# Kernel tuning notes

Hardware: AMD Instinct MI355X
Metric: run time of the kernel (lower is better)

## Reference

```python
import jax, jax.numpy as jnp
import numpy as np
import math

B, S, OBS, ACT = 64, 256, 96, 29
D, H, L, FF = 512, 8, 8, 2048
HD = D // H
EPS = 1e-5

def _ln(x, g, b):
    m = jnp.mean(x, axis=-1, keepdims=True)
    v = jnp.mean((x - m) ** 2, axis=-1, keepdims=True)
    return (x - m) * jax.lax.rsqrt(v + EPS) * g + b

def _pos_encoding():
    pos = jnp.arange(S, dtype=jnp.float32)[:, None]
    div = jnp.exp(jnp.arange(0, D, 2, dtype=jnp.float32) * (-math.log(10000.0) / D))
    pe = jnp.zeros((S, D), dtype=jnp.float32)
    pe = pe.at[:, 0::2].set(jnp.sin(pos * div))
    pe = pe.at[:, 1::2].set(jnp.cos(pos * div))
    return pe

def setup_inputs() -> dict:
    key = jax.random.key(0)
    ks = iter(jax.random.split(key, 64))
    def w(shape, scale=0.02):
        return jax.random.normal(next(ks), shape, dtype=jnp.float32) * scale
    inp = {
        "observations": jax.random.normal(next(ks), (B, S, OBS), dtype=jnp.float32),
        "W_in": w((OBS, D)), "b_in": jnp.zeros((D,)),
        "g_in": jnp.ones((D,)), "be_in": jnp.zeros((D,)),
        "Wq": w((L, D, D)), "bq": jnp.zeros((L, D)),
        "Wk": w((L, D, D)), "bk": jnp.zeros((L, D)),
        "Wv": w((L, D, D)), "bv": jnp.zeros((L, D)),
        "Wo": w((L, D, D)), "bo": jnp.zeros((L, D)),
        "g1": jnp.ones((L, D)), "be1": jnp.zeros((L, D)),
        "W1": w((L, D, FF)), "b1": jnp.zeros((L, FF)),
        "W2": w((L, FF, D)), "b2": jnp.zeros((L, D)),
        "g2": jnp.ones((L, D)), "be2": jnp.zeros((L, D)),
        "Wp1": w((D, D // 2)), "bp1": jnp.zeros((D // 2,)),
        "gp1": jnp.ones((D // 2,)), "bep1": jnp.zeros((D // 2,)),
        "Wp2": w((D // 2, D // 4)), "bp2": jnp.zeros((D // 4,)),
        "gp2": jnp.ones((D // 4,)), "bep2": jnp.zeros((D // 4,)),
        "Wp3": w((D // 4, ACT)), "bp3": jnp.zeros((ACT,)),
        "action_scale": jnp.ones((ACT,)), "action_bias": jnp.zeros((ACT,)),
    }
    return inp

def _forward(observations, W_in, b_in, g_in, be_in, Wq, bq, Wk, bk, Wv, bv, Wo, bo,
             g1, be1, W1, b1, W2, b2, g2, be2,
             Wp1, bp1, gp1, bep1, Wp2, bp2, gp2, bep2, Wp3, bp3,
             action_scale, action_bias):
    gelu = lambda x: jax.nn.gelu(x, approximate=False)
    # input projection + LN + GELU (dropout = identity in eval)
    x = gelu(_ln(observations @ W_in + b_in, g_in, be_in))
    x = x + _pos_encoding()[None, :, :]  # [B,S,D]
    scale = 1.0 / math.sqrt(HD)
    for l in range(L):
        q = (x @ Wq[l] + bq[l]).reshape(B, S, H, HD)
        k = (x @ Wk[l] + bk[l]).reshape(B, S, H, HD)
        v = (x @ Wv[l] + bv[l]).reshape(B, S, H, HD)
        scores = jnp.einsum('bqhd,bkhd->bhqk', q, k) * scale
        attn = jax.nn.softmax(scores, axis=-1)
        o = jnp.einsum('bhqk,bkhd->bqhd', attn, v).reshape(B, S, D)
        x = _ln(x + (o @ Wo[l] + bo[l]), g1[l], be1[l])
        h = gelu(x @ W1[l] + b1[l])
        x = _ln(x + (h @ W2[l] + b2[l]), g2[l], be2[l])
    y = gelu(_ln(x @ Wp1 + bp1, gp1, bep1))
    y = gelu(_ln(y @ Wp2 + bp2, gp2, bep2))
    actions = jnp.tanh(y @ Wp3 + bp3)
    return actions * action_scale + action_bias

def reference(observations, W_in, b_in, g_in, be_in, Wq, bq, Wk, bk, Wv, bv, Wo, bo,
              g1, be1, W1, b1, W2, b2, g2, be2,
              Wp1, bp1, gp1, bep1, Wp2, bp2, gp2, bep2, Wp3, bp3,
              action_scale, action_bias):
    return _forward(observations, W_in, b_in, g_in, be_in, Wq, bq, Wk, bk, Wv, bv, Wo, bo,
                    g1, be1, W1, b1, W2, b2, g2, be2,
                    Wp1, bp1, gp1, bep1, Wp2, bp2, gp2, bep2, Wp3, bp3,
                    action_scale, action_bias)
```

## Files before the change

kernel.cpp:

```cpp
#include <hip/hip_runtime.h>

typedef unsigned short u16;
typedef unsigned int u32;
typedef __attribute__((ext_vector_type(8))) __bf16 bf16x8;
typedef __attribute__((ext_vector_type(4))) float f32x4;
typedef __attribute__((ext_vector_type(2))) float f32x2;

#define B_ 64
#define S_ 256
#define OBS_ 96
#define ACT_ 29
#define D_ 512
#define H_ 8
#define L_ 8
#define FF_ 2048
#define HD_ 64
#define NTOK (B_ * S_)
#define QKV3 (3 * D_)

__device__ __forceinline__ u16 f2bf(float f) {
    __bf16 h = (__bf16)f;
    u16 u; __builtin_memcpy(&u, &h, 2); return u;
}
__device__ __forceinline__ float bf2f(u16 h) {
    return __uint_as_float(((u32)h) << 16);
}
__device__ __forceinline__ u16 f2h(float f) {
    _Float16 h = (_Float16)f;
    u16 u; __builtin_memcpy(&u, &h, 2); return u;
}
__device__ __forceinline__ float h2f(u16 u) {
    _Float16 h; __builtin_memcpy(&h, &u, 2); return (float)h;
}
__device__ __forceinline__ float gelu_f(float x) {
    const float k1 = 2.3022121f;
    const float k2 = 0.10294451f;
    float x2 = x * x;
    float arg = x * __builtin_fmaf(x2, k2, k1);
    float e = exp2f(arg);
    float r = __builtin_amdgcn_rcpf(1.0f + e);
    return __builtin_fmaf(-x, r, x);
}
__device__ __forceinline__ f32x2 gelu2(f32x2 x) {
    const float k1 = 2.3022121f;
    const float k2 = 0.10294451f;
    f32x2 x2 = x * x;
    f32x2 arg = x * (x2 * k2 + k1);
    f32x2 e;
    e.x = exp2f(arg.x);
    e.y = exp2f(arg.y);
    f32x2 one_e = e + 1.0f;
    f32x2 r;
    r.x = __builtin_amdgcn_rcpf(one_e.x);
    r.y = __builtin_amdgcn_rcpf(one_e.y);
    return x - x * r;
}
__device__ __forceinline__ void gld_lds16(const u16* g, u16* l) {
    __builtin_amdgcn_global_load_lds(
        (const __attribute__((address_space(1))) unsigned int*)g,
        (__attribute__((address_space(3))) unsigned int*)l, 16, 0, 0);
}

__global__ __launch_bounds__(256) void transpose_bf16_kernel(
    const float* __restrict__ src, u16* __restrict__ dst, int K, int N,
    size_t srcStride, size_t dstStride)
{
    __shared__ float tile[32][33];
    int n0 = blockIdx.x * 32, k0 = blockIdx.y * 32;
    const float* s = src + (size_t)blockIdx.z * srcStride;
    u16* d = dst + (size_t)blockIdx.z * dstStride;
    int tx = threadIdx.x, ty = threadIdx.y;
    for (int i = 0; i < 32; i += 8)
        tile[ty + i][tx] = s[(size_t)(k0 + ty + i) * N + n0 + tx];
    __syncthreads();
    for (int i = 0; i < 32; i += 8)
        d[(size_t)(n0 + ty + i) * K + k0 + tx] = f2bf(tile[tx][ty + i]);
}

__global__ __launch_bounds__(256) void concat_bias_kernel(
    const float* __restrict__ bq, const float* __restrict__ bk,
    const float* __restrict__ bv, float* __restrict__ dst)
{
    int i = blockIdx.x * 256 + threadIdx.x;
    int l = i / QKV3, r = i - l * QKV3;
    float v;
    if (r < D_)            v = bq[l * D_ + r];
    else if (r < 2 * D_)   v = bk[l * D_ + r - D_];
    else                   v = bv[l * D_ + r - 2 * D_];
    dst[i] = v;
}

__global__ __launch_bounds__(256) void in_gemm_kernel(
    const float* __restrict__ obs, const float* __restrict__ Win,
    const float* __restrict__ b_in, float* __restrict__ outp)
{
    __shared__ float As[OBS_][68];
    __shared__ float Bs[OBS_][68];
    int m0 = blockIdx.y * 64, n0 = blockIdx.x * 64;
    int t = threadIdx.x;
    #pragma unroll
    for (int i = 0; i < 24; i++) {
        int idx = i * 256 + t;
        int m = idx / OBS_, kk = idx - m * OBS_;
        As[kk][m] = obs[(size_t)(m0 + m) * OBS_ + kk];
    }
    #pragma unroll
    for (int i = 0; i < 24; i++) {
        int idx = i * 256 + t;
        int kk = idx >> 6, n = idx & 63;
        Bs[kk][n] = Win[(size_t)kk * D_ + n0 + n];
    }
    __syncthreads();
    int tm = t >> 4, tn = t & 15;
    float acc[4][4] = {};
    for (int kk = 0; kk < OBS_; kk++) {
        float4 a = *(const float4*)&As[kk][tm * 4];
        float4 b = *(const float4*)&Bs[kk][tn * 4];
        const float av[4] = {a.x, a.y, a.z, a.w};
        const float bv[4] = {b.x, b.y, b.z, b.w};
        #pragma unroll
        for (int r = 0; r < 4; r++)
            #pragma unroll
            for (int c = 0; c < 4; c++) acc[r][c] += av[r] * bv[c];
    }
    #pragma unroll
    for (int r = 0; r < 4; r++)
        #pragma unroll
        for (int c = 0; c < 4; c++) {
            int col = n0 + tn * 4 + c;
            outp[(size_t)(m0 + tm * 4 + r) * D_ + col] = acc[r][c] + b_in[col];
        }
}

template <int EPI, int TN, bool SPLITK>
__global__ __launch_bounds__(256, 2) void gemm_bt_kernel(
    const u16* __restrict__ A, const u16* __restrict__ BT,
    const float* __restrict__ bias, void* __restrict__ C,
    void* __restrict__ C2, int M, int N, int K, int kLen)
{
    constexpr int NI = TN / 32;
    constexpr int NB = TN / 32;
    constexpr int BUFSZ = 128 * 64 + TN * 64;
    __shared__ __align__(16) u16 smem[2 * BUFSZ];
    int bx = blockIdx.x;
    int m0 = (bx & 127) * 128, n0 = (bx >> 7) * TN;
    int z = SPLITK ? blockIdx.z : 0;
    int kStart = z * kLen;
    int t = threadIdx.x;
    int lane = t & 63, w = t >> 6;
    int wm = w >> 1, wn = w & 1;
    int l15 = lane & 15, quad = lane >> 4;

    int offC[4]; int ci8[4];
    #pragma unroll
    for (int i = 0; i < 4; i++) {
        int ci = t + i * 256;
        int r = ci >> 3, s = ci & 7, gc = s ^ (r & 7);
        offC[i] = r * K + gc * 8;
        ci8[i] = ci * 8;
    }
    const u16* Abase = A + (size_t)m0 * K + kStart;
    const u16* Bbase = BT + (size_t)n0 * K + kStart;

    int aoff[2][4], boff[2][NI];
    #pragma unroll
    for (int kh = 0; kh < 2; kh++) {
        #pragma unroll
        for (int mi = 0; mi < 4; mi++) {
            int row = wm * 64 + mi * 16 + l15;
            aoff[kh][mi] = row * 64 + (((kh * 4 + quad) ^ (row & 7)) * 8);
        }
        #pragma unroll
        for (int ni = 0; ni < NI; ni++) {
            int row = wn * (TN / 2) + ni * 16 + l15;
            boff[kh][ni] = row * 64 + (((kh * 4 + quad) ^ (row & 7)) * 8);
        }
    }

    f32x4 acc[4][NI];
    f32x4 zero = {0.f, 0.f, 0.f, 0.f};
    #pragma unroll
    for (int mi = 0; mi < 4; mi++)
        #pragma unroll
        for (int ni = 0; ni < NI; ni++) acc[mi][ni] = zero;

    auto stage = [&](int buf, int kt) {
        const u16* Ab = Abase + kt * 64;
        const u16* Bb = Bbase + kt * 64;
        u16* dstA = smem + buf * BUFSZ;
        u16* dstB = dstA + 128 * 64;
        #pragma unroll
        for (int i = 0; i < 4; i++) gld_lds16(Ab + offC[i], dstA + ci8[i]);
        #pragma unroll
        for (int i = 0; i < NB; i++) gld_lds16(Bb + offC[i], dstB + ci8[i]);
    };

    int nk = kLen >> 6;
    stage(0, 0);
    for (int kt = 0; kt < nk; ++kt) {
        int cur = kt & 1;
        __syncthreads();
        if (kt + 1 < nk) stage(cur ^ 1, kt + 1);
        const u16* As = smem + cur * BUFSZ;
        const u16* Bs = As + 128 * 64;
        #pragma unroll
        for (int kh = 0; kh < 2; kh++) {
            bf16x8 a[4], b[NI];
            #pragma unroll
            for (int mi = 0; mi < 4; mi++)
                a[mi] = *(const bf16x8*)&As[aoff[kh][mi]];
            #pragma unroll
            for (int ni = 0; ni < NI; ni++)
                b[ni] = *(const bf16x8*)&Bs[boff[kh][ni]];
            #pragma unroll
            for (int mi = 0; mi < 4; mi++)
                #pragma unroll
                for (int ni = 0; ni < NI; ni++)
                    acc[mi][ni] = __builtin_amdgcn_mfma_f32_16x16x32_bf16(
                        a[mi], b[ni], acc[mi][ni], 0, 0, 0);
        }
    }

    bool partial = SPLITK && (z == 1);
    if (EPI == 2) {
        #pragma unroll
        for (int ni = 0; ni < NI; ni++) {
            int col = n0 + wn * (TN / 2) + ni * 16 + l15;
            float bv = partial ? 0.f : bias[col];
            #pragma unroll
            for (int mi = 0; mi < 4; mi++) {
                int rbase = m0 + wm * 64 + mi * 16 + quad * 4;
                f32x4 v = acc[mi][ni];
                #pragma unroll
                for (int r = 0; r < 4; r++)
                    ((float*)C)[(size_t)(rbase + r) * N + col] = v[r] + bv;
            }
        }
    } else {
        __syncthreads();
        u16* Ct = smem;
        #pragma unroll
        for (int ni = 0; ni < NI; ni++) {
            int colt = wn * (TN / 2) + ni * 16 + l15;
            float bv = partial ? 0.f : bias[n0 + colt];
            #pragma unroll
            for (int mi = 0; mi < 4; mi++) {
                int rbase = wm * 64 + mi * 16 + quad * 4;
                f32x4 v = acc[mi][ni];
                f32x2 y01 = {v[0], v[1]};
                f32x2 y23 = {v[2], v[3]};
                y01 = y01 + bv;
                y23 = y23 + bv;
                if (EPI == 1) { y01 = gelu2(y01); y23 = gelu2(y23); }
                const float ys[4] = {y01.x, y01.y, y23.x, y23.y};
                #pragma unroll
                for (int r = 0; r < 4; r++) {
                    u16 hv = (EPI == 3) ? f2h(ys[r]) : f2bf(ys[r]);
                    int row = rbase + r;
                    int cc = colt >> 3;
                    Ct[row * TN + (((cc ^ (row & 7)) * 8) | (colt & 7))] = hv;
                }
            }
        }
        __syncthreads();
        u16* dst = partial ? (u16*)C2 : (u16*)C;
        constexpr int CPR = TN / 8;
        #pragma unroll
        for (int i = 0; i < TN / 16; i++) {
            int ch = t + i * 256;
            int row = ch / CPR, cc = ch % CPR;
            uint4 vv = *(const uint4*)&Ct[row * TN + ((cc ^ (row & 7)) * 8)];
            *(uint4*)(dst + (size_t)(m0 + row) * N + n0 + cc * 8) = vv;
        }
    }
}

__global__ __launch_bounds__(256) void attn_kernel(
    const u16* __restrict__ qkv, u16* __restrict__ o)
{
    __shared__ __align__(16) u16 kvs[S_ * HD_];
    __shared__ __align__(16) u16 P[4 * 16 * S_];
    int bx = blockIdx.x;
    int qc = bx & 3;
    int h = (bx >> 2) & 7;
    int b = bx >> 5;
    int t = threadIdx.x;
    int lane = t & 63, w = t >> 6;
    int l15 = lane & 15, quad = lane >> 4;
    size_t rowb = (size_t)b * S_;

    {
        const u16* src = qkv + (rowb + t) * QKV3 + D_ + h * HD_;
        int sw = t & 7;
        #pragma unroll
        for (int j = 0; j < 8; j++)
            *(uint4*)&kvs[t * HD_ + ((j ^ sw) * 8)] = *(const uint4*)(src + j * 8);
    }
    bf16x8 aQ[2];
    {
        int qrow = qc * 64 + w * 16 + l15;
        const u16* src = qkv + (rowb + qrow) * QKV3 + h * HD_ + quad * 8;
        aQ[0] = *(const bf16x8*)(src);
        aQ[1] = *(const bf16x8*)(src + 32);
    }
    __syncthreads();

    f32x4 sc[16];
    #pragma unroll
    for (int nc = 0; nc < 16; nc++) {
        f32x4 acc = {0.f, 0.f, 0.f, 0.f};
        int row = nc * 16 + l15;
        int s0 = quad ^ (row & 7);
        bf16x8 b0 = *(const bf16x8*)&kvs[row * HD_ + s0 * 8];
        bf16x8 b1 = *(const bf16x8*)&kvs[row * HD_ + (s0 ^ 4) * 8];
        acc = __builtin_amdgcn_mfma_f32_16x16x32_bf16(aQ[0], b0, acc, 0, 0, 0);
        acc = __builtin_amdgcn_mfma_f32_16x16x32_bf16(aQ[1], b1, acc, 0, 0, 0);
        sc[nc] = acc;
    }
    const float scale = 0.125f;
    float rmax[4], rinv[4];
    #pragma unroll
    for (int r = 0; r < 4; r++) {
        float mx = -1e30f;
        #pragma unroll
        for (int nc = 0; nc < 16; nc++) mx = fmaxf(mx, sc[nc][r]);
        for (int off = 1; off < 16; off <<= 1) mx = fmaxf(mx, __shfl_xor(mx, off));
        rmax[r] = mx * scale;
    }
    #pragma unroll
    for (int r = 0; r < 4; r++) {
        float sum = 0.f;
        #pragma unroll
        for (int nc = 0; nc < 16; nc++) {
            float p = __expf(sc[nc][r] * scale - rmax[r]);
            sc[nc][r] = p;
            sum += p;
        }
        for (int off = 1; off < 16; off <<= 1) sum += __shfl_xor(sum, off);
        rinv[r] = 1.0f / sum;
    }
    #pragma unroll
    for (int nc = 0; nc < 16; nc++)
        #pragma unroll
        for (int r = 0; r < 4; r++) {
            int prow = quad * 4 + r;
            int col = nc * 16 + l15;
            int slot = (col >> 3) ^ (prow & 7);
            P[w * 4096 + prow * 256 + slot * 8 + (col & 7)] = f2bf(sc[nc][r]);
        }
    __syncthreads();

    {
        const u16* src = qkv + (rowb + t) * QKV3 + 2 * D_ + h * HD_;
        int chunkc = t >> 3, bytec = t & 7;
        #pragma unroll
        for (int dj = 0; dj < 8; dj++) {
            uint4 x = *(const uint4*)(src + dj * 8);
            const u16* xs = (const u16*)&x;
            #pragma unroll
            for (int i = 0; i < 8; i++) {
                int vrow = dj * 8 + i;
                kvs[vrow * 256 + ((chunkc ^ (vrow & 7)) * 8) + bytec] = xs[i];
            }
        }
    }
    __syncthreads();

    f32x4 accO[4];
    f32x4 zero = {0.f, 0.f, 0.f, 0.f};
    #pragma unroll
    for (int nt = 0; nt < 4; nt++) accO[nt] = zero;
    for (int ks = 0; ks < 8; ks++) {
        int ch = ks * 4 + quad;
        bf16x8 aP = *(const bf16x8*)&P[w * 4096 + l15 * 256 + ((ch ^ (l15 & 7)) * 8)];
        #pragma unroll
        for (int nt = 0; nt < 4; nt++) {
            int vrow = nt * 16 + l15;
            bf16x8 bV = *(const bf16x8*)&kvs[vrow * 256 + ((ch ^ (vrow & 7)) * 8)];
            accO[nt] = __builtin_amdgcn_mfma_f32_16x16x32_bf16(aP, bV, accO[nt], 0, 0, 0);
        }
    }
    __syncthreads();
    u16* Ot = P;
    #pragma unroll
    for (int nt = 0; nt < 4; nt++)
        #pragma unroll
        for (int r = 0; r < 4; r++) {
            int row = w * 16 + quad * 4 + r;
            int col = nt * 16 + l15;
            int cc = col >> 3;
            Ot[row * 64 + (((cc ^ (row & 7)) * 8) | (col & 7))] =
                f2bf(accO[nt][r] * rinv[r]);
        }
    __syncthreads();
    #pragma unroll
    for (int i = 0; i < 2; i++) {
        int ch = t + i * 256;
        int row = ch >> 3, cc = ch & 7;
        uint4 vv = *(const uint4*)&Ot[row * 64 + ((cc ^ (row & 7)) * 8)];
        *(uint4*)(o + (rowb + qc * 64 + row) * D_ + h * HD_ + cc * 8) = vv;
    }
}

template <int WIDTH, int INK, bool RES, bool GELU, bool PE, bool SUM2>
__global__ __launch_bounds__(256) void ln_kernel(
    const void* __restrict__ in, const void* __restrict__ in2,
    const u16* __restrict__ res,
    const float* __restrict__ g, const float* __restrict__ b,
    u16* __restrict__ out)
{
    constexpr int T = WIDTH / 4;
    constexpr int R = 256 / T;
    __shared__ float rs[R][2], rq[R][2];
    int t = threadIdx.x;
    int r = t / T, j = t % T;
    int row = blockIdx.x * R + r;
    size_t base = (size_t)row * WIDTH + j * 4;
    float v[4];
    if (INK == 0) {
        float4 x = *(const float4*)((const float*)in + base);
        v[0] = x.x; v[1] = x.y; v[2] = x.z; v[3] = x.w;
    } else {
        uint2 x = *(const uint2*)((const u16*)in + base);
        const u16* xs = (const u16*)&x;
        #pragma unroll
        for (int i = 0; i < 4; i++) v[i] = h2f(xs[i]);
    }
    if (SUM2) {
        if (INK == 0) {
            float4 x = *(const float4*)((const float*)in2 + base);
            v[0] += x.x; v[1] += x.y; v[2] += x.z; v[3] += x.w;
        } else {
            uint2 x = *(const uint2*)((const u16*)in2 + base);
            const u16* xs = (const u16*)&x;
            #pragma unroll
            for (int i = 0; i < 4; i++) v[i] += h2f(xs[i]);
        }
    }
    if (RES) {
        uint2 x = *(const uint2*)(res + base);
        const u16* xs = (const u16*)&x;
        #pragma unroll
        for (int i = 0; i < 4; i++) v[i] += bf2f(xs[i]);
    }
    float sm = v[0] + v[1] + v[2] + v[3];
    float sq = v[0] * v[0] + v[1] * v[1] + v[2] * v[2] + v[3] * v[3];
    if constexpr (T >= 64) {
        #pragma unroll
        for (int off = 32; off; off >>= 1) {
            sm += __shfl_xor(sm, off);
            sq += __shfl_xor(sq, off);
        }
    } else {
        #pragma unroll
        for (int off = 16; off; off >>= 1) {
            sm += __shfl_xor(sm, off, 32);
            sq += __shfl_xor(sq, off, 32);
        }
    }
    if constexpr (T == 128) {
        if ((t & 63) == 0) { rs[r][(t >> 6) & 1] = sm; rq[r][(t >> 6) & 1] = sq; }
        __syncthreads();
        sm = rs[r][0] + rs[r][1];
        sq = rq[r][0] + rq[r][1];
    }
    float mean = sm / (float)WIDTH;
    float var = sq / (float)WIDTH - mean * mean;
    float rstd = rsqrtf(var + 1e-5f);
    float4 gv = *(const float4*)(g + j * 4);
    float4 bv = *(const float4*)(b + j * 4);
    const float gs[4] = {gv.x, gv.y, gv.z, gv.w};
    const float bs[4] = {bv.x, bv.y, bv.z, bv.w};
    u16 o4[4];
    #pragma unroll
    for (int i = 0; i < 4; i++) {
        float y = (v[i] - mean) * rstd * gs[i] + bs[i];
        if (GELU) y = gelu_f(y);
        if (PE) {
            const float c = -9.210340371976184f / (float)D_;
            int s = row & (S_ - 1);
            int col = j * 4 + i;
            int i2 = col >> 1;
            float ang = (float)s * __expf((float)(2 * i2) * c);
            y += (col & 1) ? __cosf(ang) : __sinf(ang);
        }
        o4[i] = f2bf(y);
    }
    uint2 ov;
    ov.x = (u32)o4[0] | ((u32)o4[1] << 16);
    ov.y = (u32)o4[2] | ((u32)o4[3] << 16);
    *(uint2*)(out + base) = ov;
}

__global__ __launch_bounds__(256) void head_kernel(
    const u16* __restrict__ y2, const float* __restrict__ W,
    const float* __restrict__ bias, const float* __restrict__ scl,
    const float* __restrict__ bs, float* __restrict__ out)
{
    __shared__ float Ws[128 * ACT_];
    __shared__ u16 Ys[8 * 128];
    int t = threadIdx.x;
    for (int i = t; i < 128 * ACT_; i += 256) Ws[i] = W[i];
    int r0 = blockIdx.x * 8;
    for (int i = t; i < 8 * 128; i += 256) Ys[i] = y2[(size_t)r0 * 128 + i];
    __syncthreads();
    int lr = t >> 5, c = t & 31;
    if (c < ACT_) {
        float acc = bias[c];
        for (int kk = 0; kk < 128; kk++)
            acc += bf2f(Ys[lr * 128 + kk]) * Ws[kk * ACT_ + c];
        float y = tanhf(acc);
        out[(size_t)(r0 + lr) * ACT_ + c] = y * scl[c] + bs[c];
    }
}

extern "C" void kernel_launch(void* const* d_in, const int* in_sizes, int n_in,
                              void* d_out, int out_size, void* d_ws, size_t ws_size,
                              hipStream_t stream)
{
    const float* obs   = (const float*)d_in[0];
    const float* W_in  = (const float*)d_in[1];
    const float* b_in  = (const float*)d_in[2];
    const float* g_in  = (const float*)d_in[3];
    const float* be_in = (const float*)d_in[4];
    const float* Wq  = (const float*)d_in[5];
    const float* bq  = (const float*)d_in[6];
    const float* Wk  = (const float*)d_in[7];
    const float* bk  = (const float*)d_in[8];
    const float* Wv  = (const float*)d_in[9];
    const float* bv  = (const float*)d_in[10];
    const float* Wo  = (const float*)d_in[11];
    const float* bo  = (const float*)d_in[12];
    const float* g1  = (const float*)d_in[13];
    const float* be1 = (const float*)d_in[14];
    const float* W1  = (const float*)d_in[15];
    const float* b1  = (const float*)d_in[16];
    const float* W2  = (const float*)d_in[17];
    const float* b2  = (const float*)d_in[18];
    const float* g2  = (const float*)d_in[19];
    const float* be2 = (const float*)d_in[20];
    const float* Wp1  = (const float*)d_in[21];
    const float* bp1  = (const float*)d_in[22];
    const float* gp1  = (const float*)d_in[23];
    const float* bep1 = (const float*)d_in[24];
    const float* Wp2  = (const float*)d_in[25];
    const float* bp2  = (const float*)d_in[26];
    const float* gp2  = (const float*)d_in[27];
    const float* bep2 = (const float*)d_in[28];
    const float* Wp3  = (const float*)d_in[29];
    const float* bp3  = (const float*)d_in[30];
    const float* ascl = (const float*)d_in[31];
    const float* abias = (const float*)d_in[32];

    char* ws = (char*)d_ws;
    size_t off = 0;
    auto alloc = [&](size_t bytes) {
        void* p = ws + off;
        off += (bytes + 255) & ~(size_t)255;
        return p;
    };
    u16* WQKVT = (u16*)alloc((size_t)L_ * QKV3 * D_ * 2);
    u16* WOT   = (u16*)alloc((size_t)L_ * D_ * D_ * 2);
    u16* W1T   = (u16*)alloc((size_t)L_ * D_ * FF_ * 2);
    u16* W2T   = (u16*)alloc((size_t)L_ * FF_ * D_ * 2);
    u16* WP1T  = (u16*)alloc((size_t)D_ * (D_ / 2) * 2);
    u16* WP2T  = (u16*)alloc((size_t)(D_ / 2) * (D_ / 4) * 2);
    float* bqkv = (float*)alloc((size_t)L_ * QKV3 * 4);
    u16* x_bf = (u16*)alloc((size_t)NTOK * D_ * 2);
    float* tmp = (float*)alloc((size_t)NTOK * D_ * 4);
    char* regionA = (char*)alloc((size_t)NTOK * FF_ * 2);
    size_t base_need = off;
    char* tmp2 = ws + base_need;
    bool split = (ws_size >= base_need + (size_t)NTOK * D_ * 2);
    (void)in_sizes; (void)n_in; (void)out_size;

    u16* qkvbuf = (u16*)(regionA);
    u16* obuf = (u16*)(regionA + (size_t)NTOK * QKV3 * 2);
    u16* hbuf = (u16*)(regionA);
    u16* y1_bf = (u16*)(regionA);
    u16* y2_bf = (u16*)(regionA + (32u << 20));

    dim3 tb(32, 8);
    size_t DD = (size_t)D_ * D_;
    transpose_bf16_kernel<<<dim3(16, 16, L_), tb, 0, stream>>>(
        Wq, WQKVT, D_, D_, DD, (size_t)QKV3 * D_);
    transpose_bf16_kernel<<<dim3(16, 16, L_), tb, 0, stream>>>(
        Wk, WQKVT + DD, D_, D_, DD, (size_t)QKV3 * D_);
    transpose_bf16_kernel<<<dim3(16, 16, L_), tb, 0, stream>>>(
        Wv, WQKVT + 2 * DD, D_, D_, DD, (size_t)QKV3 * D_);
    transpose_bf16_kernel<<<dim3(16, 16, L_), tb, 0, stream>>>(
        Wo, WOT, D_, D_, DD, DD);
    transpose_bf16_kernel<<<dim3(64, 16, L_), tb, 0, stream>>>(
        W1, W1T, D_, FF_, (size_t)D_ * FF_, (size_t)D_ * FF_);
    transpose_bf16_kernel<<<dim3(16, 64, L_), tb, 0, stream>>>(
        W2, W2T, FF_, D_, (size_t)D_ * FF_, (size_t)D_ * FF_);
    transpose_bf16_kernel<<<dim3(8, 16, 1), tb, 0, stream>>>(
        Wp1, WP1T, D_, D_ / 2, 0, 0);
    transpose_bf16_kernel<<<dim3(4, 8, 1), tb, 0, stream>>>(
        Wp2, WP2T, D_ / 2, D_ / 4, 0, 0);
    concat_bias_kernel<<<L_ * QKV3 / 256, 256, 0, stream>>>(bq, bk, bv, bqkv);

    in_gemm_kernel<<<dim3(D_ / 64, NTOK / 64), 256, 0, stream>>>(
        obs, W_in, b_in, tmp);
    ln_kernel<D_, 0, false, true, true, false><<<NTOK / 2, 256, 0, stream>>>(
        tmp, nullptr, nullptr, g_in, be_in, x_bf);

    const int MG = NTOK / 128;
    for (int l = 0; l < L_; l++) {
        const u16* wqkvt = WQKVT + (size_t)l * QKV3 * D_;
        const u16* wot = WOT + (size_t)l * DD;
        const u16* w1t = W1T + (size_t)l * D_ * FF_;
        const u16* w2t = W2T + (size_t)l * FF_ * D_;

        gemm_bt_kernel<0, 128, false><<<MG * (QKV3 / 128), 256, 0, stream>>>(
            x_bf, wqkvt, bqkv + l * QKV3, qkvbuf, nullptr, NTOK, QKV3, D_, D_);
        attn_kernel<<<B_ * H_ * (S_ / 64), 256, 0, stream>>>(qkvbuf, obuf);
        if (split) {
            gemm_bt_kernel<3, 128, true><<<dim3(MG * 4, 1, 2), 256, 0, stream>>>(
                obuf, wot, bo + l * D_, tmp, tmp2, NTOK, D_, D_, D_ / 2);
            ln_kernel<D_, 1, true, false, false, true><<<NTOK / 2, 256, 0, stream>>>(
                tmp, tmp2, x_bf, g1 + l * D_, be1 + l * D_, x_bf);
        } else {
            gemm_bt_kernel<2, 128, false><<<MG * 4, 256, 0, stream>>>(
                obuf, wot, bo + l * D_, tmp, nullptr, NTOK, D_, D_, D_);
            ln_kernel<D_, 0, true, false, false, false><<<NTOK / 2, 256, 0, stream>>>(
                tmp, nullptr, x_bf, g1 + l * D_, be1 + l * D_, x_bf);
        }
        gemm_bt_kernel<1, 128, false><<<MG * (FF_ / 128), 256, 0, stream>>>(
            x_bf, w1t, b1 + l * FF_, hbuf, nullptr, NTOK, FF_, D_, D_);
        if (split) {
            gemm_bt_kernel<3, 128, true><<<dim3(MG * 4, 1, 2), 256, 0, stream>>>(
                hbuf, w2t, b2 + l * D_, tmp, tmp2, NTOK, D_, FF_, FF_ / 2);
            ln_kernel<D_, 1, true, false, false, true><<<NTOK / 2, 256, 0, stream>>>(
                tmp, tmp2, x_bf, g2 + l * D_, be2 + l * D_, x_bf);
        } else {
            gemm_bt_kernel<2, 128, false><<<MG * 4, 256, 0, stream>>>(
                hbuf, w2t, b2 + l * D_, tmp, nullptr, NTOK, D_, FF_, FF_);
            ln_kernel<D_, 0, true, false, false, false><<<NTOK / 2, 256, 0, stream>>>(
                tmp, nullptr, x_bf, g2 + l * D_, be2 + l * D_, x_bf);
        }
    }

    if (split) {
        gemm_bt_kernel<3, 64, true><<<dim3(MG * 4, 1, 2), 256, 0, stream>>>(
            x_bf, WP1T, bp1, tmp, tmp2, NTOK, D_ / 2, D_, D_ / 2);
        ln_kernel<D_ / 2, 1, false, true, false, true><<<NTOK / 4, 256, 0, stream>>>(
            tmp, tmp2, nullptr, gp1, bep1, y1_bf);
        gemm_bt_kernel<3, 64, true><<<dim3(MG * 2, 1, 2), 256, 0, stream>>>(
            y1_bf, WP2T, bp2, tmp, tmp2, NTOK, D_ / 4, D_ / 2, D_ / 4);
        ln_kernel<D_ / 4, 1, false, true, false, true><<<NTOK / 8, 256, 0, stream>>>(
            tmp, tmp2, nullptr, gp2, bep2, y2_bf);
    } else {
        gemm_bt_kernel<2, 64, false><<<MG * 4, 256, 0, stream>>>(
            x_bf, WP1T, bp1, tmp, nullptr, NTOK, D_ / 2, D_, D_);
        ln_kernel<D_ / 2, 0, false, true, false, false><<<NTOK / 4, 256, 0, stream>>>(
            tmp, nullptr, nullptr, gp1, bep1, y1_bf);
        gemm_bt_kernel<2, 64, false><<<MG * 2, 256, 0, stream>>>(
            y1_bf, WP2T, bp2, tmp, nullptr, NTOK, D_ / 4, D_ / 2, D_ / 2);
        ln_kernel<D_ / 4, 0, false, true, false, false><<<NTOK / 8, 256, 0, stream>>>(
            tmp, nullptr, nullptr, gp2, bep2, y2_bf);
    }
    head_kernel<<<NTOK / 8, 256, 0, stream>>>(
        y2_bf, Wp3, bp3, ascl, abias, (float*)d_out);
}
```

Baseline: 2.063 ms.

## Halve GEMM K-tile to 32 with new LDS swizzle and raise occupancy to 3 blocks

The bf16 MFMA GEMM now stages 32-wide K slices instead of 64, which halves shared memory per block. It switches to a 4-chunk XOR swizzle that matches the new row width, and raises launch_bounds min blocks from 2 to 3 per CU. The aim is more resident waves to hide global-load latency. In exchange the loop runs twice as many iterations with a __syncthreads each, has less MFMA work per barrier, and gets a tighter register budget that may cause spills.

```diff
diff --git a/kernel.cpp b/kernel.cpp
--- a/kernel.cpp
+++ b/kernel.cpp
@@ -133,15 +133,16 @@
 }
 
 template <int EPI, int TN, bool SPLITK>
-__global__ __launch_bounds__(256, 2) void gemm_bt_kernel(
+__global__ __launch_bounds__(256, 3) void gemm_bt_kernel(
     const u16* __restrict__ A, const u16* __restrict__ BT,
     const float* __restrict__ bias, void* __restrict__ C,
     void* __restrict__ C2, int M, int N, int K, int kLen)
 {
     constexpr int NI = TN / 32;
-    constexpr int NB = TN / 32;
-    constexpr int BUFSZ = 128 * 64 + TN * 64;
-    __shared__ __align__(16) u16 smem[2 * BUFSZ];
+    constexpr int BCH = TN / 64;
+    constexpr int ABUF = 128 * 32;
+    constexpr int BBUF = TN * 32;
+    __shared__ __align__(16) u16 smem[2 * ABUF + 2 * BBUF];
     int bx = blockIdx.x;
     int m0 = (bx & 127) * 128, n0 = (bx >> 7) * TN;
     int z = SPLITK ? blockIdx.z : 0;
@@ -151,30 +152,32 @@
     int wm = w >> 1, wn = w & 1;
     int l15 = lane & 15, quad = lane >> 4;
 
-    int offC[4]; int ci8[4];
-    #pragma unroll
-    for (int i = 0; i < 4; i++) {
+    int offA[2], offB[BCH];
+    #pragma unroll
+    for (int i = 0; i < 2; i++) {
         int ci = t + i * 256;
-        int r = ci >> 3, s = ci & 7, gc = s ^ (r & 7);
-        offC[i] = r * K + gc * 8;
-        ci8[i] = ci * 8;
-    }
-    const u16* Abase = A + (size_t)m0 * K + kStart;
-    const u16* Bbase = BT + (size_t)n0 * K + kStart;
-
-    int aoff[2][4], boff[2][NI];
-    #pragma unroll
-    for (int kh = 0; kh < 2; kh++) {
-        #pragma unroll
-        for (int mi = 0; mi < 4; mi++) {
-            int row = wm * 64 + mi * 16 + l15;
-            aoff[kh][mi] = row * 64 + (((kh * 4 + quad) ^ (row & 7)) * 8);
-        }
-        #pragma unroll
-        for (int ni = 0; ni < NI; ni++) {
-            int row = wn * (TN / 2) + ni * 16 + l15;
-            boff[kh][ni] = row * 64 + (((kh * 4 + quad) ^ (row & 7)) * 8);
-        }
+        int r = ci >> 2, s = ci & 3, gc = s ^ ((r ^ (r >> 2)) & 3);
+        offA[i] = r * K + gc * 8;
+    }
+    #pragma unroll
+    for (int i = 0; i < BCH; i++) {
+        int ci = t + i * 256;
+        int r = ci >> 2, s = ci & 3, gc = s ^ ((r ^ (r >> 2)) & 3);
+        offB[i] = r * K + gc * 8;
+    }
+    const u16* Ag = A + (size_t)m0 * K + kStart;
+    const u16* Bg = BT + (size_t)n0 * K + kStart;
+
+    int aoff[4], boff[NI];
+    #pragma unroll
+    for (int mi = 0; mi < 4; mi++) {
+        int row = wm * 64 + mi * 16 + l15;
+        aoff[mi] = row * 32 + ((quad ^ ((row ^ (row >> 2)) & 3)) * 8);
+    }
+    #pragma unroll
+    for (int ni = 0; ni < NI; ni++) {
+        int row = wn * (TN / 2) + ni * 16 + l15;
+        boff[ni] = row * 32 + ((quad ^ ((row ^ (row >> 2)) & 3)) * 8);
     }
 
     f32x4 acc[4][NI];
@@ -185,40 +188,37 @@
         for (int ni = 0; ni < NI; ni++) acc[mi][ni] = zero;
 
     auto stage = [&](int buf, int kt) {
-        const u16* Ab = Abase + kt * 64;
-        const u16* Bb = Bbase + kt * 64;
-        u16* dstA = smem + buf * BUFSZ;
-        u16* dstB = dstA + 128 * 64;
-        #pragma unroll
-        for (int i = 0; i < 4; i++) gld_lds16(Ab + offC[i], dstA + ci8[i]);
-        #pragma unroll
-        for (int i = 0; i < NB; i++) gld_lds16(Bb + offC[i], dstB + ci8[i]);
+        const u16* Ab = Ag + kt * 32;
+        const u16* Bb = Bg + kt * 32;
+        u16* dA = smem + buf * ABUF;
+        u16* dB = smem + 2 * ABUF + buf * BBUF;
+        #pragma unroll
+        for (int i = 0; i < 2; i++) gld_lds16(Ab + offA[i], dA + (t + i * 256) * 8);
+        #pragma unroll
+        for (int i = 0; i < BCH; i++) gld_lds16(Bb + offB[i], dB + (t + i * 256) * 8);
     };
 
-    int nk = kLen >> 6;
+    int nk = kLen >> 5;
     stage(0, 0);
     for (int kt = 0; kt < nk; ++kt) {
         int cur = kt & 1;
         __syncthreads();
         if (kt + 1 < nk) stage(cur ^ 1, kt + 1);
-        const u16* As = smem + cur * BUFSZ;
-        const u16* Bs = As + 128 * 64;
-        #pragma unroll
-        for (int kh = 0; kh < 2; kh++) {
-            bf16x8 a[4], b[NI];
-            #pragma unroll
-            for (int mi = 0; mi < 4; mi++)
-                a[mi] = *(const bf16x8*)&As[aoff[kh][mi]];
+        const u16* As = smem + cur * ABUF;
+        const u16* Bs = smem + 2 * ABUF + cur * BBUF;
+        bf16x8 a[4], b[NI];
+        #pragma unroll
+        for (int mi = 0; mi < 4; mi++)
+            a[mi] = *(const bf16x8*)&As[aoff[mi]];
+        #pragma unroll
+        for (int ni = 0; ni < NI; ni++)
+            b[ni] = *(const bf16x8*)&Bs[boff[ni]];
+        #pragma unroll
+        for (int mi = 0; mi < 4; mi++)
             #pragma unroll
             for (int ni = 0; ni < NI; ni++)
-                b[ni] = *(const bf16x8*)&Bs[boff[kh][ni]];
-            #pragma unroll
-            for (int mi = 0; mi < 4; mi++)
-                #pragma unroll
-                for (int ni = 0; ni < NI; ni++)
-                    acc[mi][ni] = __builtin_amdgcn_mfma_f32_16x16x32_bf16(
-                        a[mi], b[ni], acc[mi][ni], 0, 0, 0);
-        }
+                acc[mi][ni] = __builtin_amdgcn_mfma_f32_16x16x32_bf16(
+                    a[mi], b[ni], acc[mi][ni], 0, 0, 0);
     }
 
     bool partial = SPLITK && (z == 1);
```

After: 2.060 ms. No clear change (-0.1%).
